# Optimization experiments

Measured on AMD Instinct MI355X. Metric: run time of the kernel, lower is better.

## Reference

```python
import jax, jax.numpy as jnp
import numpy as np

TEMPERATURE = 0.07
EPS = 1e-8


def setup_inputs() -> dict:
    key = jax.random.key(0)
    k1, k2 = jax.random.split(key)
    anchor_embeddings = jax.random.normal(k1, (4096, 512), dtype=jnp.float32)
    positive_embeddings = jax.random.normal(k2, (8192, 512), dtype=jnp.float32)
    return {
        "anchor_embeddings": anchor_embeddings,
        "positive_embeddings": positive_embeddings,
    }


def reference(anchor_embeddings, positive_embeddings):
    B, D = anchor_embeddings.shape
    P = positive_embeddings.shape[0] // B

    # L2 normalize (F.normalize, p=2, dim=1)
    a = anchor_embeddings / jnp.linalg.norm(anchor_embeddings, axis=1, keepdims=True)
    p = positive_embeddings / jnp.linalg.norm(positive_embeddings, axis=1, keepdims=True)
    p = p.reshape(B, P, D)

    # temperature-scaled similarities
    pos = jnp.einsum("bd,bpd->bp", a, p) / TEMPERATURE            # [B, P]
    aa = jnp.matmul(a, a.T) / TEMPERATURE                          # [B, B]

    # sum over in-batch negatives (exclude diagonal self-similarity)
    exp_aa = jnp.exp(aa)
    neg_sumexp = jnp.sum(exp_aa, axis=1) - jnp.diagonal(exp_aa)    # [B]

    # loss_ij = -log(exp(pos_ij) / (exp(pos_ij) + neg_sumexp_i + 1e-8))
    exp_pos = jnp.exp(pos)
    denom = exp_pos + neg_sumexp[:, None] + EPS
    losses = -jnp.log(exp_pos / denom)                             # [B, P]
    return jnp.mean(losses)
```

## Files before the change

### kernel.cpp

```cpp
#include <hip/hip_runtime.h>
#include <hip/hip_bf16.h>

typedef __bf16  bf16x8 __attribute__((ext_vector_type(8)));
typedef float   f32x4  __attribute__((ext_vector_type(4)));

constexpr int   Bsz   = 4096;
constexpr int   D     = 512;
constexpr int   Pn    = 2;
constexpr float INV_T = 1.0f / 0.07f;
constexpr float EPSF  = 1e-8f;

constexpr int NT = 528;
constexpr int POS_BLOCKS = Bsz / 4;

#define GLOBAL_AS __attribute__((address_space(1)))
#define LDS_AS    __attribute__((address_space(3)))

__device__ __forceinline__ void stage16(const void* g, void* l) {
  __builtin_amdgcn_global_load_lds((const GLOBAL_AS unsigned int*)g,
                                   (LDS_AS unsigned int*)l, 16, 0, 0);
}

__global__ __launch_bounds__(256) void norm_kernel(
    const float* __restrict__ A, __hip_bfloat16* __restrict__ Abf,
    float* __restrict__ neg, float* __restrict__ out) {
  const int lane = threadIdx.x & 63;
  const int wave = threadIdx.x >> 6;
  const int row  = blockIdx.x * 4 + wave;
  const int gid  = blockIdx.x * 256 + threadIdx.x;
  if (gid < Bsz) neg[gid] = 0.0f;
  if (gid == 0)  out[0]   = 0.0f;

  const float4* ap = reinterpret_cast<const float4*>(A + (size_t)row * D + lane * 8);
  const float4 v0 = ap[0];
  const float4 v1 = ap[1];
  float ss = v0.x*v0.x + v0.y*v0.y + v0.z*v0.z + v0.w*v0.w
           + v1.x*v1.x + v1.y*v1.y + v1.z*v1.z + v1.w*v1.w;
#pragma unroll
  for (int m = 1; m < 64; m <<= 1) ss += __shfl_xor(ss, m);
  const float inv = rsqrtf(ss);

  union { __hip_bfloat16 h[8]; uint4 u; } o;
  o.h[0] = __float2bfloat16(v0.x * inv);
  o.h[1] = __float2bfloat16(v0.y * inv);
  o.h[2] = __float2bfloat16(v0.z * inv);
  o.h[3] = __float2bfloat16(v0.w * inv);
  o.h[4] = __float2bfloat16(v1.x * inv);
  o.h[5] = __float2bfloat16(v1.y * inv);
  o.h[6] = __float2bfloat16(v1.z * inv);
  o.h[7] = __float2bfloat16(v1.w * inv);
  reinterpret_cast<uint4*>(Abf + (size_t)row * D + lane * 8)[0] = o.u;
}

#define BK 32

__global__ __launch_bounds__(256) void negsum_pos_kernel(
    const __hip_bfloat16* __restrict__ Abf, float* __restrict__ neg,
    const float* __restrict__ A, const float* __restrict__ Pm,
    float* __restrict__ pos) {
  const int tid  = threadIdx.x;
  const int lane = tid & 63;
  const int wave = tid >> 6;

  if (blockIdx.x >= NT) {
    const int b = (blockIdx.x - NT) * 4 + wave;

    const float4* ap  = reinterpret_cast<const float4*>(A  + (size_t)b * D + lane * 8);
    const float4* p0p = reinterpret_cast<const float4*>(Pm + (size_t)(2 * b) * D + lane * 8);
    const float4* p1p = reinterpret_cast<const float4*>(Pm + (size_t)(2 * b + 1) * D + lane * 8);
    const float4 a0 = ap[0],  a1 = ap[1];
    const float4 q0 = p0p[0], q1 = p0p[1];
    const float4 r0 = p1p[0], r1 = p1p[1];

    float daa  = a0.x*a0.x + a0.y*a0.y + a0.z*a0.z + a0.w*a0.w
               + a1.x*a1.x + a1.y*a1.y + a1.z*a1.z + a1.w*a1.w;
    float dpp0 = q0.x*q0.x + q0.y*q0.y + q0.z*q0.z + q0.w*q0.w
               + q1.x*q1.x + q1.y*q1.y + q1.z*q1.z + q1.w*q1.w;
    float dpp1 = r0.x*r0.x + r0.y*r0.y + r0.z*r0.z + r0.w*r0.w
               + r1.x*r1.x + r1.y*r1.y + r1.z*r1.z + r1.w*r1.w;
    float dap0 = a0.x*q0.x + a0.y*q0.y + a0.z*q0.z + a0.w*q0.w
               + a1.x*q1.x + a1.y*q1.y + a1.z*q1.z + a1.w*q1.w;
    float dap1 = a0.x*r0.x + a0.y*r0.y + a0.z*r0.z + a0.w*r0.w
               + a1.x*r1.x + a1.y*r1.y + a1.z*r1.z + a1.w*r1.w;
#pragma unroll
    for (int m = 1; m < 64; m <<= 1) {
      daa  += __shfl_xor(daa,  m);
      dpp0 += __shfl_xor(dpp0, m);
      dpp1 += __shfl_xor(dpp1, m);
      dap0 += __shfl_xor(dap0, m);
      dap1 += __shfl_xor(dap1, m);
    }
    if (lane == 0) {
      const float ia = rsqrtf(daa);
      pos[2 * b]     = dap0 * ia * rsqrtf(dpp0) * INV_T;
      pos[2 * b + 1] = dap1 * ia * rsqrtf(dpp1) * INV_T;
    }
    return;
  }

  __shared__ __attribute__((aligned(16))) ushort At[128 * BK];
  __shared__ __attribute__((aligned(16))) ushort Bt[128 * BK];

  const int i = blockIdx.x;
  int by = (int)((sqrtf(8.0f * (float)i + 1.0f) - 1.0f) * 0.5f);
  while ((by + 1) * (by + 2) / 2 <= i) ++by;
  while (by * (by + 1) / 2 > i) --by;
  const int bx = i - by * (by + 1) / 2;

  const int brow = bx * 128;
  const int bcol = by * 128;
  const bool offdiag = (bx != by);

  const int waveM = wave >> 1;
  const int waveN = wave & 1;

  const int fr  = lane & 15;
  const int kch = lane >> 4;
  const int ckr = (kch ^ ((fr >> 1) & 3)) * 8;

  const int srow = lane >> 2;
  const int sck  = ((lane & 3) ^ ((lane >> 3) & 3));

  f32x4 acc[4][4] = {};

  for (int k0 = 0; k0 < D; k0 += BK) {
#pragma unroll
    for (int t = 0; t < 2; ++t) {
      const int r0 = wave * 32 + t * 16;
      stage16(&Abf[(size_t)(brow + r0 + srow) * D + k0 + sck * 8], &At[r0 * BK]);
      stage16(&Abf[(size_t)(bcol + r0 + srow) * D + k0 + sck * 8], &Bt[r0 * BK]);
    }
    __syncthreads();

    bf16x8 af[4], bfv[4];
#pragma unroll
    for (int m = 0; m < 4; ++m)
      af[m] = *reinterpret_cast<const bf16x8*>(
          &At[(waveM * 64 + m * 16 + fr) * BK + ckr]);
#pragma unroll
    for (int n = 0; n < 4; ++n)
      bfv[n] = *reinterpret_cast<const bf16x8*>(
          &Bt[(waveN * 64 + n * 16 + fr) * BK + ckr]);

#pragma unroll
    for (int m = 0; m < 4; ++m)
#pragma unroll
      for (int n = 0; n < 4; ++n)
        acc[m][n] = __builtin_amdgcn_mfma_f32_16x16x32_bf16(
            af[m], bfv[n], acc[m][n], 0, 0, 0);
    __syncthreads();
  }

  const int q = lane >> 4;
  float colsum[4] = {0.f, 0.f, 0.f, 0.f};
#pragma unroll
  for (int m = 0; m < 4; ++m) {
#pragma unroll
    for (int r = 0; r < 4; ++r) {
      const int grow = brow + waveM * 64 + m * 16 + q * 4 + r;
      float rs = 0.0f;
#pragma unroll
      for (int n = 0; n < 4; ++n) {
        const int gcol = bcol + waveN * 64 + n * 16 + fr;
        const float e = (grow != gcol) ? __expf(acc[m][n][r] * INV_T) : 0.0f;
        rs += e;
        colsum[n] += e;
      }
      rs += __shfl_xor(rs, 1);
      rs += __shfl_xor(rs, 2);
      rs += __shfl_xor(rs, 4);
      rs += __shfl_xor(rs, 8);
      if (fr == 0) atomicAdd(&neg[grow], rs);
    }
  }
  if (offdiag) {
#pragma unroll
    for (int n = 0; n < 4; ++n) {
      float cs = colsum[n];
      cs += __shfl_xor(cs, 16);
      cs += __shfl_xor(cs, 32);
      if (q == 0) atomicAdd(&neg[bcol + waveN * 64 + n * 16 + fr], cs);
    }
  }
}

__global__ __launch_bounds__(256) void loss_kernel(
    const float* __restrict__ pos, const float* __restrict__ neg,
    float* __restrict__ out) {
  const int i = blockIdx.x * 256 + threadIdx.x;
  const int b = i >> 1;
  const float po = pos[i];
  float s = logf(expf(po) + neg[b] + EPSF) - po;
#pragma unroll
  for (int m = 1; m < 64; m <<= 1) s += __shfl_xor(s, m);
  __shared__ float wsum[4];
  if ((threadIdx.x & 63) == 0) wsum[threadIdx.x >> 6] = s;
  __syncthreads();
  if (threadIdx.x == 0)
    atomicAdd(out, (wsum[0] + wsum[1] + wsum[2] + wsum[3]) * (1.0f / (Bsz * Pn)));
}

extern "C" void kernel_launch(void* const* d_in, const int* in_sizes, int n_in,
                              void* d_out, int out_size, void* d_ws, size_t ws_size,
                              hipStream_t stream) {
  const float* A  = (const float*)d_in[0];
  const float* Pm = (const float*)d_in[1];
  float* out = (float*)d_out;

  __hip_bfloat16* Abf = (__hip_bfloat16*)d_ws;
  float* pos = (float*)((char*)d_ws + (size_t)Bsz * D * 2);
  float* neg = pos + Bsz * Pn;

  norm_kernel<<<Bsz / 4, 256, 0, stream>>>(A, Abf, neg, out);
  negsum_pos_kernel<<<NT + POS_BLOCKS, 256, 0, stream>>>(Abf, neg, A, Pm, pos);
  loss_kernel<<<32, 256, 0, stream>>>(pos, neg, out);
}
```

Measured before the change: 33.03 us.

## Double-buffer LDS tiles to overlap global loads with MFMA in Gram GEMM

Adds a second pair of LDS tile buffers so the next K-slice is staged via global_load_lds while the current slice is read into registers and multiplied. This cuts one barrier per K step and hides global memory latency behind MFMA work. The cost is double the LDS per block (32KB), which may lower occupancy, and the K loop is now fully unrolled, which grows code size.

```diff
diff --git a/kernel.cpp b/kernel.cpp
--- a/kernel.cpp
+++ b/kernel.cpp
@@ -58,6 +58,11 @@
     const __hip_bfloat16* __restrict__ Abf, float* __restrict__ neg,
     const float* __restrict__ A, const float* __restrict__ Pm,
     float* __restrict__ pos) {
+  __shared__ __attribute__((aligned(16))) ushort At0[128 * BK];
+  __shared__ __attribute__((aligned(16))) ushort Bt0[128 * BK];
+  __shared__ __attribute__((aligned(16))) ushort At1[128 * BK];
+  __shared__ __attribute__((aligned(16))) ushort Bt1[128 * BK];
+
   const int tid  = threadIdx.x;
   const int lane = tid & 63;
   const int wave = tid >> 6;
@@ -98,9 +103,6 @@
     return;
   }
 
-  __shared__ __attribute__((aligned(16))) ushort At[128 * BK];
-  __shared__ __attribute__((aligned(16))) ushort Bt[128 * BK];
-
   const int i = blockIdx.x;
   int by = (int)((sqrtf(8.0f * (float)i + 1.0f) - 1.0f) * 0.5f);
   while ((by + 1) * (by + 2) / 2 <= i) ++by;
@@ -123,33 +125,45 @@
 
   f32x4 acc[4][4] = {};
 
-  for (int k0 = 0; k0 < D; k0 += BK) {
-#pragma unroll
-    for (int t = 0; t < 2; ++t) {
-      const int r0 = wave * 32 + t * 16;
-      stage16(&Abf[(size_t)(brow + r0 + srow) * D + k0 + sck * 8], &At[r0 * BK]);
-      stage16(&Abf[(size_t)(bcol + r0 + srow) * D + k0 + sck * 8], &Bt[r0 * BK]);
-    }
-    __syncthreads();
-
-    bf16x8 af[4], bfv[4];
-#pragma unroll
-    for (int m = 0; m < 4; ++m)
-      af[m] = *reinterpret_cast<const bf16x8*>(
-          &At[(waveM * 64 + m * 16 + fr) * BK + ckr]);
-#pragma unroll
-    for (int n = 0; n < 4; ++n)
-      bfv[n] = *reinterpret_cast<const bf16x8*>(
-          &Bt[(waveN * 64 + n * 16 + fr) * BK + ckr]);
-
-#pragma unroll
-    for (int m = 0; m < 4; ++m)
-#pragma unroll
-      for (int n = 0; n < 4; ++n)
-        acc[m][n] = __builtin_amdgcn_mfma_f32_16x16x32_bf16(
-            af[m], bfv[n], acc[m][n], 0, 0, 0);
-    __syncthreads();
-  }
+#pragma unroll
+  for (int t = 0; t < 2; ++t) {
+    const int r0 = wave * 32 + t * 16;
+    stage16(&Abf[(size_t)(brow + r0 + srow) * D + sck * 8], &At0[r0 * BK]);
+    stage16(&Abf[(size_t)(bcol + r0 + srow) * D + sck * 8], &Bt0[r0 * BK]);
+  }
+  __syncthreads();
+
+#define GEMM_STEP(CA, CB, NA, NB, KS)                                        \
+  {                                                                          \
+    bf16x8 af[4], bfv[4];                                                    \
+    _Pragma("unroll") for (int m = 0; m < 4; ++m)                            \
+      af[m] = *reinterpret_cast<const bf16x8*>(                              \
+          &CA[(waveM * 64 + m * 16 + fr) * BK + ckr]);                       \
+    _Pragma("unroll") for (int n = 0; n < 4; ++n)                            \
+      bfv[n] = *reinterpret_cast<const bf16x8*>(                             \
+          &CB[(waveN * 64 + n * 16 + fr) * BK + ckr]);                       \
+    if ((KS) < D) {                                                          \
+      _Pragma("unroll") for (int t = 0; t < 2; ++t) {                        \
+        const int r0 = wave * 32 + t * 16;                                   \
+        stage16(&Abf[(size_t)(brow + r0 + srow) * D + (KS) + sck * 8],       \
+                &NA[r0 * BK]);                                               \
+        stage16(&Abf[(size_t)(bcol + r0 + srow) * D + (KS) + sck * 8],       \
+                &NB[r0 * BK]);                                               \
+      }                                                                      \
+    }                                                                        \
+    _Pragma("unroll") for (int m = 0; m < 4; ++m)                            \
+      _Pragma("unroll") for (int n = 0; n < 4; ++n)                          \
+        acc[m][n] = __builtin_amdgcn_mfma_f32_16x16x32_bf16(                 \
+            af[m], bfv[n], acc[m][n], 0, 0, 0);                              \
+    __syncthreads();                                                         \
+  }
+
+#pragma unroll
+  for (int k0 = 0; k0 < D; k0 += 2 * BK) {
+    GEMM_STEP(At0, Bt0, At1, Bt1, k0 + BK);
+    GEMM_STEP(At1, Bt1, At0, Bt0, k0 + 2 * BK);
+  }
+#undef GEMM_STEP
 
   const int q = lane >> 4;
   float colsum[4] = {0.f, 0.f, 0.f, 0.f};
```

Result: slower. 40.78 us (+23.5%).

## Load MFMA operands directly from global memory instead of LDS staging

Applied to the files above, without the earlier changes.

Drops the LDS tiles, the global_load_lds staging and both per-iteration barriers from the Gram-matrix tiles. Each wave now reads its bf16 fragments straight from global memory (served by L2/L1) inside a fully unrolled K loop. This removes synchronisation and LDS traffic, but every wave re-fetches data that the two waves sharing a row or column block would otherwise have shared, which raises global and cache load traffic. The fully unrolled loop may also raise register pressure.

```diff
diff --git a/kernel.cpp b/kernel.cpp
--- a/kernel.cpp
+++ b/kernel.cpp
@@ -11,15 +11,7 @@
 constexpr float EPSF  = 1e-8f;
 
 constexpr int NT = 528;
-constexpr int POS_BLOCKS = Bsz / 4;
-
-#define GLOBAL_AS __attribute__((address_space(1)))
-#define LDS_AS    __attribute__((address_space(3)))
-
-__device__ __forceinline__ void stage16(const void* g, void* l) {
-  __builtin_amdgcn_global_load_lds((const GLOBAL_AS unsigned int*)g,
-                                   (LDS_AS unsigned int*)l, 16, 0, 0);
-}
+constexpr int POS_BLOCKS = 1024;
 
 __global__ __launch_bounds__(256) void norm_kernel(
     const float* __restrict__ A, __hip_bfloat16* __restrict__ Abf,
@@ -51,8 +43,6 @@
   o.h[7] = __float2bfloat16(v1.w * inv);
   reinterpret_cast<uint4*>(Abf + (size_t)row * D + lane * 8)[0] = o.u;
 }
-
-#define BK 32
 
 __global__ __launch_bounds__(256) void negsum_pos_kernel(
     const __hip_bfloat16* __restrict__ Abf, float* __restrict__ neg,
@@ -98,9 +88,6 @@
     return;
   }
 
-  __shared__ __attribute__((aligned(16))) ushort At[128 * BK];
-  __shared__ __attribute__((aligned(16))) ushort Bt[128 * BK];
-
   const int i = blockIdx.x;
   int by = (int)((sqrtf(8.0f * (float)i + 1.0f) - 1.0f) * 0.5f);
   while ((by + 1) * (by + 2) / 2 <= i) ++by;
@@ -116,31 +103,21 @@
 
   const int fr  = lane & 15;
   const int kch = lane >> 4;
-  const int ckr = (kch ^ ((fr >> 1) & 3)) * 8;
 
-  const int srow = lane >> 2;
-  const int sck  = ((lane & 3) ^ ((lane >> 3) & 3));
+  const __hip_bfloat16* abase = Abf + (size_t)(brow + waveM * 64 + fr) * D + kch * 8;
+  const __hip_bfloat16* bbase = Abf + (size_t)(bcol + waveN * 64 + fr) * D + kch * 8;
 
   f32x4 acc[4][4] = {};
 
-  for (int k0 = 0; k0 < D; k0 += BK) {
 #pragma unroll
-    for (int t = 0; t < 2; ++t) {
-      const int r0 = wave * 32 + t * 16;
-      stage16(&Abf[(size_t)(brow + r0 + srow) * D + k0 + sck * 8], &At[r0 * BK]);
-      stage16(&Abf[(size_t)(bcol + r0 + srow) * D + k0 + sck * 8], &Bt[r0 * BK]);
-    }
-    __syncthreads();
-
+  for (int k0 = 0; k0 < D; k0 += 32) {
     bf16x8 af[4], bfv[4];
 #pragma unroll
     for (int m = 0; m < 4; ++m)
-      af[m] = *reinterpret_cast<const bf16x8*>(
-          &At[(waveM * 64 + m * 16 + fr) * BK + ckr]);
+      af[m] = *reinterpret_cast<const bf16x8*>(abase + (size_t)m * 16 * D + k0);
 #pragma unroll
     for (int n = 0; n < 4; ++n)
-      bfv[n] = *reinterpret_cast<const bf16x8*>(
-          &Bt[(waveN * 64 + n * 16 + fr) * BK + ckr]);
+      bfv[n] = *reinterpret_cast<const bf16x8*>(bbase + (size_t)n * 16 * D + k0);
 
 #pragma unroll
     for (int m = 0; m < 4; ++m)
@@ -148,7 +125,6 @@
       for (int n = 0; n < 4; ++n)
         acc[m][n] = __builtin_amdgcn_mfma_f32_16x16x32_bf16(
             af[m], bfv[n], acc[m][n], 0, 0, 0);
-    __syncthreads();
   }
 
   const int q = lane >> 4;
```

Measured after the change: 61.65 us. +86.7%, slower.
